# Optimization experiments

Hardware: AMD Instinct MI355X
Metric: run time of the kernel (lower is better)

Reference implementation:

```python
import jax, jax.numpy as jnp
import numpy as np

T = 4        # number of atom types (len(atomtype))
N = 65536    # number of atoms
D = 256      # nl[0] == nl[1] == nl[2]
EPS = 1e-5   # LayerNorm eps (torch default)


def setup_inputs() -> dict:
    key = jax.random.key(0)
    ks = jax.random.split(key, 16)
    s = 1.0 / np.sqrt(D)  # xavier-ish scale
    f32 = jnp.float32
    return {
        "density": jax.random.normal(ks[0], (N, D), f32),
        "species": jax.random.randint(ks[1], (N,), 0, T, jnp.int32),
        # first Linear(nl[0], nl[1]) per type
        "W0": jax.random.normal(ks[2], (T, D, D), f32) * s,
        "b0": jnp.zeros((T, D), f32),
        # ResBlock: actfun (Relu_like: alpha*silu(Wx+b)), LayerNorm, Linear
        "Wa": jax.random.normal(ks[3], (T, D, D), f32) * s,
        "ba": jnp.zeros((T, D), f32),
        "alpha_a": jnp.ones((T, D), f32),
        "gamma": jnp.ones((T, D), f32),
        "beta_ln": jnp.zeros((T, D), f32),
        "Wl": jax.random.normal(ks[4], (T, D, D), f32) * s,
        "bl": jnp.zeros((T, D), f32),
        # tail actfun(nl[nhid-1], nl[nhid])
        "Wf": jax.random.normal(ks[5], (T, D, D), f32) * s,
        "bf": jnp.zeros((T, D), f32),
        "alpha_f": jnp.ones((T, D), f32),
        # output Linear(nl[nhid], outputneuron=1); randomized (zero-init is degenerate for testing)
        "Wo": jax.random.normal(ks[6], (T, 1, D), f32) * s,
        "bo": jnp.zeros((T, 1), f32),
    }


def _layernorm(x, g, b):
    mu = jnp.mean(x, axis=-1, keepdims=True)
    var = jnp.mean((x - mu) ** 2, axis=-1, keepdims=True)
    return g * (x - mu) * jax.lax.rsqrt(var + EPS) + b


def _expert(W0, b0, Wa, ba, alpha_a, gamma, beta_ln, Wl, bl, Wf, bf, alpha_f, Wo, bo, density):
    # Sequential: Linear -> ResBlock(actfun, LN, Linear) -> actfun -> Linear
    x = density @ W0.T + b0                       # [N, D]
    h = alpha_a * jax.nn.silu(x @ Wa.T + ba)      # Relu_like actfun
    h = _layernorm(h, gamma, beta_ln)
    x = x + (h @ Wl.T + bl)                       # residual add
    x = alpha_f * jax.nn.silu(x @ Wf.T + bf)
    return x @ Wo.T + bo                          # [N, 1]


def reference(density, species, W0, b0, Wa, ba, alpha_a, gamma, beta_ln, Wl, bl, Wf, bf, alpha_f, Wo, bo):
    # Apply every type's expert to all atoms, then pick the row for each atom's type.
    # Same math as the torch gather/scatter dispatch (every species value is in [0, T)).
    y_all = jax.vmap(_expert, in_axes=(0,) * 14 + (None,))(
        W0, b0, Wa, ba, alpha_a, gamma, beta_ln, Wl, bl, Wf, bf, alpha_f, Wo, bo, density
    )  # [T, N, 1]
    return y_all[species, jnp.arange(N)]          # [N, 1]
```

## Files before the change

kernel.cpp:

```cpp
#include <hip/hip_runtime.h>
#include <hip/hip_bf16.h>


#define D 256
#define T 4
#define MT 64
#define NTHREADS 512
#define LDSTRIDE 264
#define CSTRIDE 32

typedef __attribute__((ext_vector_type(8))) short bf16x8;
typedef __attribute__((ext_vector_type(4))) float f32x4;

__device__ __forceinline__ float bf2f(unsigned short s) {
    union { unsigned u; float f; } c;
    c.u = ((unsigned)s) << 16;
    return c.f;
}
__device__ __forceinline__ unsigned cvtpk(float a, float b) {
    unsigned r;
    asm("v_cvt_pk_bf16_f32 %0, %1, %2" : "=v"(r) : "v"(a), "v"(b));
    return r;
}
__device__ __forceinline__ float lo2f(unsigned u) { return bf2f((unsigned short)(u & 0xffffu)); }
__device__ __forceinline__ float hi2f(unsigned u) { return bf2f((unsigned short)(u >> 16)); }
__device__ __forceinline__ float silu(float v) {
    return v * __builtin_amdgcn_rcpf(1.f + __expf(-v));
}

extern "C" __global__ void k_prep(const int* __restrict__ species, int* cursors,
                                  int* __restrict__ perm, int N,
                                  const float* __restrict__ s0, const float* __restrict__ s1,
                                  const float* __restrict__ s2, const float* __restrict__ s3,
                                  unsigned short* __restrict__ d0, unsigned short* __restrict__ d1,
                                  unsigned short* __restrict__ d2, unsigned short* __restrict__ d3, int n4) {
    __shared__ int lh[T], lbase[T];
    int tid = threadIdx.x;
    if (tid < T) lh[tid] = 0;
    __syncthreads();
    int i = blockIdx.x * blockDim.x + tid;
    int t = -1, rank = 0;
    if (i < N) {
        t = species[i];
        rank = atomicAdd(&lh[t], 1);
    }
    if (i < n4) {
        float4 v;
        v = ((const float4*)s0)[i]; ((uint2*)d0)[i] = make_uint2(cvtpk(v.x, v.y), cvtpk(v.z, v.w));
        v = ((const float4*)s1)[i]; ((uint2*)d1)[i] = make_uint2(cvtpk(v.x, v.y), cvtpk(v.z, v.w));
        v = ((const float4*)s2)[i]; ((uint2*)d2)[i] = make_uint2(cvtpk(v.x, v.y), cvtpk(v.z, v.w));
        v = ((const float4*)s3)[i]; ((uint2*)d3)[i] = make_uint2(cvtpk(v.x, v.y), cvtpk(v.z, v.w));
    }
    __syncthreads();
    if (tid < T) lbase[tid] = atomicAdd(&cursors[tid * CSTRIDE], lh[tid]);
    __syncthreads();
    if (t >= 0) perm[t * N + lbase[t] + rank] = i;
}


extern "C" __global__ void __launch_bounds__(NTHREADS, 4)
fused_moe(const float* __restrict__ density,
          const int* __restrict__ perm,
          const int* __restrict__ counts,
          const unsigned short* __restrict__ W0b,
          const unsigned short* __restrict__ Wab,
          const unsigned short* __restrict__ Wlb,
          const unsigned short* __restrict__ Wfb,
          const float* __restrict__ b0g, const float* __restrict__ bag,
          const float* __restrict__ aag, const float* __restrict__ gg,
          const float* __restrict__ btg, const float* __restrict__ blg,
          const float* __restrict__ bfg, const float* __restrict__ afg,
          const float* __restrict__ Wog, const float* __restrict__ bog,
          float* __restrict__ out, int N)
{
    __shared__ unsigned short Xs[MT * LDSTRIDE];
    __shared__ float Pbias[D], Palpha[D];
    __shared__ float Pwo[D];
    __shared__ float red1[NTHREADS], red2[NTHREADS];

    const int tid = threadIdx.x;

    int c[T];
#pragma unroll
    for (int i = 0; i < T; ++i) c[i] = counts[i * CSTRIDE];
    int t = -1, tile = 0, rem = blockIdx.x;
#pragma unroll
    for (int i = 0; i < T; ++i) {
        int ti = (c[i] + MT - 1) >> 6;
        if (t < 0) {
            if (rem < ti) { t = i; tile = rem; }
            else rem -= ti;
        }
    }
    if (t < 0) return;
    const int bstart = t * N + tile * MT;
    const int nrows = min(MT, c[t] - tile * MT);

    if (tid < D) {
        Pbias[tid] = b0g[t * D + tid];
        Pwo[tid]   = Wog[t * D + tid];
    }

#pragma unroll
    for (int p = 0; p < 2; ++p) {
        int row = p * 32 + (tid >> 4);
        int cbase = (tid & 15) * 4;
        unsigned short* dst = Xs + row * LDSTRIDE;
        if (row < nrows) {
            const float* src = density + (size_t)perm[bstart + row] * D;
#pragma unroll
            for (int j = 0; j < 4; ++j) {
                int col = cbase + j * 64;
                float4 v = *(const float4*)(src + col);
                *(uint2*)(dst + col) = make_uint2(cvtpk(v.x, v.y), cvtpk(v.z, v.w));
            }
        } else {
#pragma unroll
            for (int j = 0; j < 4; ++j)
                *(uint2*)(dst + cbase + j * 64) = make_uint2(0u, 0u);
        }
    }
    __syncthreads();

    const int lane = tid & 63;
    const int w    = tid >> 6;
    const int ml   = lane & 15;
    const int qk   = (lane >> 4) * 8;
    const int qr   = (lane >> 4) * 4;

    const size_t wmat = (size_t)t * D * D;
    const unsigned short* W0t = W0b + wmat;
    const unsigned short* Wat = Wab + wmat;
    const unsigned short* Wlt = Wlb + wmat;
    const unsigned short* Wft = Wfb + wmat;

    f32x4 acc[2][4];
    const f32x4 zero4 = {0.f, 0.f, 0.f, 0.f};

    auto do_gemm = [&](const unsigned short* __restrict__ W) {
#pragma unroll
        for (int mi = 0; mi < 2; ++mi)
#pragma unroll
            for (int ni = 0; ni < 4; ++ni) acc[mi][ni] = zero4;
#pragma unroll
        for (int k0 = 0; k0 < D; k0 += 32) {
            bf16x8 a[2], b[4];
#pragma unroll
            for (int mi = 0; mi < 2; ++mi)
                a[mi] = *(const bf16x8*)(W + (size_t)(w * 32 + mi * 16 + ml) * D + k0 + qk);
#pragma unroll
            for (int ni = 0; ni < 4; ++ni)
                b[ni] = *(const bf16x8*)(Xs + (ni * 16 + ml) * LDSTRIDE + k0 + qk);
#pragma unroll
            for (int mi = 0; mi < 2; ++mi)
#pragma unroll
                for (int ni = 0; ni < 4; ++ni)
                    acc[mi][ni] = __builtin_amdgcn_mfma_f32_16x16x32_bf16(a[mi], b[ni], acc[mi][ni], 0, 0, 0);
        }
    };


    do_gemm(W0t);
    __syncthreads();
    unsigned res[2][4][2];
#pragma unroll
    for (int mi = 0; mi < 2; ++mi) {
#pragma unroll
        for (int ni = 0; ni < 4; ++ni) {
            int r0 = w * 32 + mi * 16 + qr;
            int a0 = ni * 16 + ml;
            float4 bb = *(const float4*)(Pbias + r0);
            unsigned p01 = cvtpk(acc[mi][ni][0] + bb.x, acc[mi][ni][1] + bb.y);
            unsigned p23 = cvtpk(acc[mi][ni][2] + bb.z, acc[mi][ni][3] + bb.w);
            res[mi][ni][0] = p01;
            res[mi][ni][1] = p23;
            *(uint2*)(Xs + a0 * LDSTRIDE + r0) = make_uint2(p01, p23);
        }
    }
    __syncthreads();

    if (tid < D) {
        Pbias[tid]  = bag[t * D + tid];
        Palpha[tid] = aag[t * D + tid];
    }
    do_gemm(Wat);
    __syncthreads();
#pragma unroll
    for (int mi = 0; mi < 2; ++mi) {
#pragma unroll
        for (int ni = 0; ni < 4; ++ni) {
            int r0 = w * 32 + mi * 16 + qr;
            int a0 = ni * 16 + ml;
            float4 bb = *(const float4*)(Pbias + r0);
            float4 aa = *(const float4*)(Palpha + r0);
            float v0 = aa.x * silu(acc[mi][ni][0] + bb.x);
            float v1 = aa.y * silu(acc[mi][ni][1] + bb.y);
            float v2 = aa.z * silu(acc[mi][ni][2] + bb.z);
            float v3 = aa.w * silu(acc[mi][ni][3] + bb.w);
            *(uint2*)(Xs + a0 * LDSTRIDE + r0) = make_uint2(cvtpk(v0, v1), cvtpk(v2, v3));
        }
    }
    __syncthreads();

    {
        if (tid < D) {
            Pbias[tid]  = gg[t * D + tid];
            Palpha[tid] = btg[t * D + tid];
        }
        int row = tid & 63, q = tid >> 6;
        const bf16x8* base = (const bf16x8*)(Xs + row * LDSTRIDE + q * 32);
        bf16x8 hv[4];
        float sum = 0.f, ssq = 0.f;
#pragma unroll
        for (int j = 0; j < 4; ++j) {
            hv[j] = base[j];
#pragma unroll
            for (int e = 0; e < 8; ++e) {
                float f = bf2f((unsigned short)hv[j][e]);
                sum += f;
                ssq = fmaf(f, f, ssq);
            }
        }
        red1[tid] = sum; red2[tid] = ssq;
        __syncthreads();
        if (tid < MT) {
            float s = 0.f, sq = 0.f;
#pragma unroll
            for (int k = 0; k < 8; ++k) { s += red1[tid + 64 * k]; sq += red2[tid + 64 * k]; }
            float mu = s * (1.f / D);
            float var = sq * (1.f / D) - mu * mu;
            red1[tid] = mu;
            red2[tid] = rsqrtf(var + 1e-5f);
        }
        __syncthreads();
        float mu = red1[row], rs = red2[row];
        unsigned short* wb = Xs + row * LDSTRIDE + q * 32;
#pragma unroll
        for (int j = 0; j < 4; ++j) {
            float n[8];
#pragma unroll
            for (int e = 0; e < 8; ++e) {
                int col = q * 32 + j * 8 + e;
                float f = bf2f((unsigned short)hv[j][e]);
                n[e] = fmaf((f - mu) * rs, Pbias[col], Palpha[col]);
            }
            uint4 o = make_uint4(cvtpk(n[0], n[1]), cvtpk(n[2], n[3]),
                                 cvtpk(n[4], n[5]), cvtpk(n[6], n[7]));
            *(uint4*)(wb + j * 8) = o;
        }
    }
    __syncthreads();

    if (tid < D) Pbias[tid] = blg[t * D + tid];
    do_gemm(Wlt);
    __syncthreads();
#pragma unroll
    for (int mi = 0; mi < 2; ++mi) {
#pragma unroll
        for (int ni = 0; ni < 4; ++ni) {
            int r0 = w * 32 + mi * 16 + qr;
            int a0 = ni * 16 + ml;
            float4 bb = *(const float4*)(Pbias + r0);
            float v0 = acc[mi][ni][0] + bb.x + lo2f(res[mi][ni][0]);
            float v1 = acc[mi][ni][1] + bb.y + hi2f(res[mi][ni][0]);
            float v2 = acc[mi][ni][2] + bb.z + lo2f(res[mi][ni][1]);
            float v3 = acc[mi][ni][3] + bb.w + hi2f(res[mi][ni][1]);
            *(uint2*)(Xs + a0 * LDSTRIDE + r0) = make_uint2(cvtpk(v0, v1), cvtpk(v2, v3));
        }
    }
    __syncthreads();

    if (tid < D) {
        Pbias[tid]  = bfg[t * D + tid];
        Palpha[tid] = afg[t * D + tid];
    }
    do_gemm(Wft);
    __syncthreads();
#pragma unroll
    for (int mi = 0; mi < 2; ++mi) {
#pragma unroll
        for (int ni = 0; ni < 4; ++ni) {
            int r0 = w * 32 + mi * 16 + qr;
            int a0 = ni * 16 + ml;
            float4 bb = *(const float4*)(Pbias + r0);
            float4 aa = *(const float4*)(Palpha + r0);
            float v0 = aa.x * silu(acc[mi][ni][0] + bb.x);
            float v1 = aa.y * silu(acc[mi][ni][1] + bb.y);
            float v2 = aa.z * silu(acc[mi][ni][2] + bb.z);
            float v3 = aa.w * silu(acc[mi][ni][3] + bb.w);
            *(uint2*)(Xs + a0 * LDSTRIDE + r0) = make_uint2(cvtpk(v0, v1), cvtpk(v2, v3));
        }
    }
    __syncthreads();

    {
        int row = tid & 63, q = tid >> 6;
        const bf16x8* base = (const bf16x8*)(Xs + row * LDSTRIDE + q * 32);
        float part = 0.f;
#pragma unroll
        for (int j = 0; j < 4; ++j) {
            bf16x8 hv = base[j];
#pragma unroll
            for (int e = 0; e < 8; ++e)
                part = fmaf(bf2f((unsigned short)hv[e]), Pwo[q * 32 + j * 8 + e], part);
        }
        red1[tid] = part;
        __syncthreads();
        if (tid < nrows) {
            float val = bog[t];
#pragma unroll
            for (int k = 0; k < 8; ++k) val += red1[tid + 64 * k];
            out[perm[bstart + tid]] = val;
        }
    }
}


extern "C" void kernel_launch(void* const* d_in, const int* in_sizes, int n_in,
                              void* d_out, int out_size, void* d_ws, size_t ws_size,
                              hipStream_t stream) {
    const float* density = (const float*)d_in[0];
    const int*   species = (const int*)d_in[1];
    const float* W0      = (const float*)d_in[2];
    const float* b0      = (const float*)d_in[3];
    const float* Wa      = (const float*)d_in[4];
    const float* ba      = (const float*)d_in[5];
    const float* alpha_a = (const float*)d_in[6];
    const float* gamma   = (const float*)d_in[7];
    const float* beta_ln = (const float*)d_in[8];
    const float* Wl      = (const float*)d_in[9];
    const float* bl      = (const float*)d_in[10];
    const float* Wf      = (const float*)d_in[11];
    const float* bfv     = (const float*)d_in[12];
    const float* alpha_f = (const float*)d_in[13];
    const float* Wo      = (const float*)d_in[14];
    const float* bo      = (const float*)d_in[15];
    float* out = (float*)d_out;
    const int N = in_sizes[1];

    char* ws = (char*)d_ws;
    int* cursors = (int*)ws;
    int* perm    = (int*)(ws + 1024);
    const size_t wsz = (size_t)T * D * D;
    unsigned short* W0b = (unsigned short*)(ws + 1024 + (size_t)T * N * 4);
    unsigned short* Wab = W0b + wsz;
    unsigned short* Wlb = Wab + wsz;
    unsigned short* Wfb = Wlb + wsz;

    hipMemsetAsync(ws, 0, 512, stream);
    int n4 = (int)(wsz / 4);
    int pb = ((N > n4 ? N : n4) + 255) / 256;
    k_prep<<<pb, 256, 0, stream>>>(species, cursors, perm, N, W0, Wa, Wl, Wf,
                                   W0b, Wab, Wlb, Wfb, n4);

    int nblocks = (N + MT - 1) / MT + T;
    fused_moe<<<nblocks, NTHREADS, 0, stream>>>(density, perm, cursors, W0b, Wab, Wlb, Wfb,
                                                b0, ba, alpha_a, gamma, beta_ln, bl, bfv, alpha_f,
                                                Wo, bo, out, N);
}
```

Baseline: 201.2 us.

## Double-buffer LDS activations, XOR-swizzle layout, preload params, prefetch weight fragments

Activations now ping-pong between two LDS buffers, which removes the barrier between each GEMM and the epilogue that overwrites its input. The padded stride is replaced by an XOR swizzle to avoid bank conflicts. All per-type bias and scale vectors are loaded into LDS once at kernel start. The first k-slice of the next layer's weights is prefetched into registers during the current epilogue. LDS use roughly doubles, from about 36 KB to about 77 KB per block, which may lower occupancy below the launch-bounds target of 4 blocks.

```diff
diff --git a/kernel.cpp b/kernel.cpp
--- a/kernel.cpp
+++ b/kernel.cpp
@@ -6,8 +6,9 @@
 #define T 4
 #define MT 64
 #define NTHREADS 512
-#define LDSTRIDE 264
 #define CSTRIDE 32
+
+#define XSW(row, col) (((row) << 8) + ((col) ^ (((row) & 7) << 3)))
 
 typedef __attribute__((ext_vector_type(8))) short bf16x8;
 typedef __attribute__((ext_vector_type(4))) float f32x4;
@@ -73,9 +74,8 @@
           const float* __restrict__ Wog, const float* __restrict__ bog,
           float* __restrict__ out, int N)
 {
-    __shared__ unsigned short Xs[MT * LDSTRIDE];
-    __shared__ float Pbias[D], Palpha[D];
-    __shared__ float Pwo[D];
+    __shared__ unsigned short Xs[2][MT * D];
+    __shared__ float Pb0[D], Pba[D], Paa[D], Pg[D], Pbt[D], Pbl[D], Pbf[D], Paf[D], Pwo[D];
     __shared__ float red1[NTHREADS], red2[NTHREADS];
 
     const int tid = threadIdx.x;
@@ -96,32 +96,6 @@
     const int bstart = t * N + tile * MT;
     const int nrows = min(MT, c[t] - tile * MT);
 
-    if (tid < D) {
-        Pbias[tid] = b0g[t * D + tid];
-        Pwo[tid]   = Wog[t * D + tid];
-    }
-
-#pragma unroll
-    for (int p = 0; p < 2; ++p) {
-        int row = p * 32 + (tid >> 4);
-        int cbase = (tid & 15) * 4;
-        unsigned short* dst = Xs + row * LDSTRIDE;
-        if (row < nrows) {
-            const float* src = density + (size_t)perm[bstart + row] * D;
-#pragma unroll
-            for (int j = 0; j < 4; ++j) {
-                int col = cbase + j * 64;
-                float4 v = *(const float4*)(src + col);
-                *(uint2*)(dst + col) = make_uint2(cvtpk(v.x, v.y), cvtpk(v.z, v.w));
-            }
-        } else {
-#pragma unroll
-            for (int j = 0; j < 4; ++j)
-                *(uint2*)(dst + cbase + j * 64) = make_uint2(0u, 0u);
-        }
-    }
-    __syncthreads();
-
     const int lane = tid & 63;
     const int w    = tid >> 6;
     const int ml   = lane & 15;
@@ -134,10 +108,45 @@
     const unsigned short* Wlt = Wlb + wmat;
     const unsigned short* Wft = Wfb + wmat;
 
+    bf16x8 pf0, pf1;
+    auto prefA = [&](const unsigned short* __restrict__ W) {
+        pf0 = *(const bf16x8*)(W + (size_t)(w * 32 + ml) * D + qk);
+        pf1 = *(const bf16x8*)(W + (size_t)(w * 32 + 16 + ml) * D + qk);
+    };
+
+    prefA(W0t);
+
+    if (tid < D) {
+        int j = t * D + tid;
+        Pb0[tid] = b0g[j]; Pba[tid] = bag[j]; Paa[tid] = aag[j];
+        Pg[tid]  = gg[j];  Pbt[tid] = btg[j]; Pbl[tid] = blg[j];
+        Pbf[tid] = bfg[j]; Paf[tid] = afg[j]; Pwo[tid] = Wog[j];
+    }
+
+#pragma unroll
+    for (int p = 0; p < 2; ++p) {
+        int row = p * 32 + (tid >> 4);
+        int cbase = (tid & 15) * 4;
+        if (row < nrows) {
+            const float* src = density + (size_t)perm[bstart + row] * D;
+#pragma unroll
+            for (int j = 0; j < 4; ++j) {
+                int col = cbase + j * 64;
+                float4 v = *(const float4*)(src + col);
+                *(uint2*)(&Xs[0][XSW(row, col)]) = make_uint2(cvtpk(v.x, v.y), cvtpk(v.z, v.w));
+            }
+        } else {
+#pragma unroll
+            for (int j = 0; j < 4; ++j)
+                *(uint2*)(&Xs[0][XSW(row, cbase + j * 64)]) = make_uint2(0u, 0u);
+        }
+    }
+    __syncthreads();
+
     f32x4 acc[2][4];
     const f32x4 zero4 = {0.f, 0.f, 0.f, 0.f};
 
-    auto do_gemm = [&](const unsigned short* __restrict__ W) {
+    auto do_gemm = [&](const unsigned short* __restrict__ W, const unsigned short* __restrict__ Xb) {
 #pragma unroll
         for (int mi = 0; mi < 2; ++mi)
 #pragma unroll
@@ -145,12 +154,15 @@
 #pragma unroll
         for (int k0 = 0; k0 < D; k0 += 32) {
             bf16x8 a[2], b[4];
-#pragma unroll
-            for (int mi = 0; mi < 2; ++mi)
-                a[mi] = *(const bf16x8*)(W + (size_t)(w * 32 + mi * 16 + ml) * D + k0 + qk);
+            if (k0 == 0) { a[0] = pf0; a[1] = pf1; }
+            else {
+#pragma unroll
+                for (int mi = 0; mi < 2; ++mi)
+                    a[mi] = *(const bf16x8*)(W + (size_t)(w * 32 + mi * 16 + ml) * D + k0 + qk);
+            }
 #pragma unroll
             for (int ni = 0; ni < 4; ++ni)
-                b[ni] = *(const bf16x8*)(Xs + (ni * 16 + ml) * LDSTRIDE + k0 + qk);
+                b[ni] = *(const bf16x8*)(Xb + XSW(ni * 16 + ml, k0 + qk));
 #pragma unroll
             for (int mi = 0; mi < 2; ++mi)
 #pragma unroll
@@ -160,8 +172,8 @@
     };
 
 
-    do_gemm(W0t);
-    __syncthreads();
+    do_gemm(W0t, Xs[0]);
+    prefA(Wat);
     unsigned res[2][4][2];
 #pragma unroll
     for (int mi = 0; mi < 2; ++mi) {
@@ -169,51 +181,42 @@
         for (int ni = 0; ni < 4; ++ni) {
             int r0 = w * 32 + mi * 16 + qr;
             int a0 = ni * 16 + ml;
-            float4 bb = *(const float4*)(Pbias + r0);
+            float4 bb = *(const float4*)(Pb0 + r0);
             unsigned p01 = cvtpk(acc[mi][ni][0] + bb.x, acc[mi][ni][1] + bb.y);
             unsigned p23 = cvtpk(acc[mi][ni][2] + bb.z, acc[mi][ni][3] + bb.w);
             res[mi][ni][0] = p01;
             res[mi][ni][1] = p23;
-            *(uint2*)(Xs + a0 * LDSTRIDE + r0) = make_uint2(p01, p23);
-        }
-    }
-    __syncthreads();
-
-    if (tid < D) {
-        Pbias[tid]  = bag[t * D + tid];
-        Palpha[tid] = aag[t * D + tid];
-    }
-    do_gemm(Wat);
-    __syncthreads();
+            *(uint2*)(&Xs[1][XSW(a0, r0)]) = make_uint2(p01, p23);
+        }
+    }
+    __syncthreads();
+
+    do_gemm(Wat, Xs[1]);
+    prefA(Wlt);
 #pragma unroll
     for (int mi = 0; mi < 2; ++mi) {
 #pragma unroll
         for (int ni = 0; ni < 4; ++ni) {
             int r0 = w * 32 + mi * 16 + qr;
             int a0 = ni * 16 + ml;
-            float4 bb = *(const float4*)(Pbias + r0);
-            float4 aa = *(const float4*)(Palpha + r0);
+            float4 bb = *(const float4*)(Pba + r0);
+            float4 aa = *(const float4*)(Paa + r0);
             float v0 = aa.x * silu(acc[mi][ni][0] + bb.x);
             float v1 = aa.y * silu(acc[mi][ni][1] + bb.y);
             float v2 = aa.z * silu(acc[mi][ni][2] + bb.z);
             float v3 = aa.w * silu(acc[mi][ni][3] + bb.w);
-            *(uint2*)(Xs + a0 * LDSTRIDE + r0) = make_uint2(cvtpk(v0, v1), cvtpk(v2, v3));
+            *(uint2*)(&Xs[0][XSW(a0, r0)]) = make_uint2(cvtpk(v0, v1), cvtpk(v2, v3));
         }
     }
     __syncthreads();
 
     {
-        if (tid < D) {
-            Pbias[tid]  = gg[t * D + tid];
-            Palpha[tid] = btg[t * D + tid];
-        }
         int row = tid & 63, q = tid >> 6;
-        const bf16x8* base = (const bf16x8*)(Xs + row * LDSTRIDE + q * 32);
         bf16x8 hv[4];
         float sum = 0.f, ssq = 0.f;
 #pragma unroll
         for (int j = 0; j < 4; ++j) {
-            hv[j] = base[j];
+            hv[j] = *(const bf16x8*)(&Xs[0][XSW(row, q * 32 + j * 8)]);
 #pragma unroll
             for (int e = 0; e < 8; ++e) {
                 float f = bf2f((unsigned short)hv[j][e]);
@@ -234,7 +237,6 @@
         }
         __syncthreads();
         float mu = red1[row], rs = red2[row];
-        unsigned short* wb = Xs + row * LDSTRIDE + q * 32;
 #pragma unroll
         for (int j = 0; j < 4; ++j) {
             float n[8];
@@ -242,64 +244,57 @@
             for (int e = 0; e < 8; ++e) {
                 int col = q * 32 + j * 8 + e;
                 float f = bf2f((unsigned short)hv[j][e]);
-                n[e] = fmaf((f - mu) * rs, Pbias[col], Palpha[col]);
+                n[e] = fmaf((f - mu) * rs, Pg[col], Pbt[col]);
             }
             uint4 o = make_uint4(cvtpk(n[0], n[1]), cvtpk(n[2], n[3]),
                                  cvtpk(n[4], n[5]), cvtpk(n[6], n[7]));
-            *(uint4*)(wb + j * 8) = o;
-        }
-    }
-    __syncthreads();
-
-    if (tid < D) Pbias[tid] = blg[t * D + tid];
-    do_gemm(Wlt);
-    __syncthreads();
+            *(uint4*)(&Xs[1][XSW(row, q * 32 + j * 8)]) = o;
+        }
+    }
+    __syncthreads();
+
+    do_gemm(Wlt, Xs[1]);
+    prefA(Wft);
 #pragma unroll
     for (int mi = 0; mi < 2; ++mi) {
 #pragma unroll
         for (int ni = 0; ni < 4; ++ni) {
             int r0 = w * 32 + mi * 16 + qr;
             int a0 = ni * 16 + ml;
-            float4 bb = *(const float4*)(Pbias + r0);
+            float4 bb = *(const float4*)(Pbl + r0);
             float v0 = acc[mi][ni][0] + bb.x + lo2f(res[mi][ni][0]);
             float v1 = acc[mi][ni][1] + bb.y + hi2f(res[mi][ni][0]);
             float v2 = acc[mi][ni][2] + bb.z + lo2f(res[mi][ni][1]);
             float v3 = acc[mi][ni][3] + bb.w + hi2f(res[mi][ni][1]);
-            *(uint2*)(Xs + a0 * LDSTRIDE + r0) = make_uint2(cvtpk(v0, v1), cvtpk(v2, v3));
-        }
-    }
-    __syncthreads();
-
-    if (tid < D) {
-        Pbias[tid]  = bfg[t * D + tid];
-        Palpha[tid] = afg[t * D + tid];
-    }
-    do_gemm(Wft);
-    __syncthreads();
+            *(uint2*)(&Xs[0][XSW(a0, r0)]) = make_uint2(cvtpk(v0, v1), cvtpk(v2, v3));
+        }
+    }
+    __syncthreads();
+
+    do_gemm(Wft, Xs[0]);
 #pragma unroll
     for (int mi = 0; mi < 2; ++mi) {
 #pragma unroll
         for (int ni = 0; ni < 4; ++ni) {
             int r0 = w * 32 + mi * 16 + qr;
             int a0 = ni * 16 + ml;
-            float4 bb = *(const float4*)(Pbias + r0);
-            float4 aa = *(const float4*)(Palpha + r0);
+            float4 bb = *(const float4*)(Pbf + r0);
+            float4 aa = *(const float4*)(Paf + r0);
             float v0 = aa.x * silu(acc[mi][ni][0] + bb.x);
             float v1 = aa.y * silu(acc[mi][ni][1] + bb.y);
             float v2 = aa.z * silu(acc[mi][ni][2] + bb.z);
             float v3 = aa.w * silu(acc[mi][ni][3] + bb.w);
-            *(uint2*)(Xs + a0 * LDSTRIDE + r0) = make_uint2(cvtpk(v0, v1), cvtpk(v2, v3));
+            *(uint2*)(&Xs[1][XSW(a0, r0)]) = make_uint2(cvtpk(v0, v1), cvtpk(v2, v3));
         }
     }
     __syncthreads();
 
     {
         int row = tid & 63, q = tid >> 6;
-        const bf16x8* base = (const bf16x8*)(Xs + row * LDSTRIDE + q * 32);
         float part = 0.f;
 #pragma unroll
         for (int j = 0; j < 4; ++j) {
-            bf16x8 hv = base[j];
+            bf16x8 hv = *(const bf16x8*)(&Xs[1][XSW(row, q * 32 + j * 8)]);
 #pragma unroll
             for (int e = 0; e < 8; ++e)
                 part = fmaf(bf2f((unsigned short)hv[e]), Pwo[q * 32 + j * 8 + e], part);
```

Result: no change. 199.0 us (-1.1%).
